# Performance work log

Measured on AMD Instinct MI355X. Metric: run time of the kernel, lower is better.

The kernel has to match this reference:

```python
import jax, jax.numpy as jnp
import numpy as np

B, W, N, L = 64, 256, 128, 64


def setup_inputs() -> dict:
    key = jax.random.key(0)
    k1, k2, k3 = jax.random.split(key, 3)
    x = jax.random.normal(k1, (B, W, L), dtype=jnp.float32)
    shapelets = jax.random.normal(k2, (N, L), dtype=jnp.float32)
    cls_w = jax.random.normal(k3, (1, N), dtype=jnp.float32) * 0.1
    cls_b = jnp.zeros((1,), dtype=jnp.float32)
    return {"x": x, "shapelets": shapelets, "cls_w": cls_w, "cls_b": cls_b}


def reference(x, shapelets, cls_w, cls_b):
    # diffs: [B, W, N, L] broadcast subtract
    diffs = x[:, :, None, :] - shapelets[None, None, :, :]
    # L2 norm over shapelet-length axis -> [B, W, N]
    discrim = jnp.sqrt(jnp.sum(diffs * diffs, axis=3))
    # min over windows -> [B, N]
    min_discrim = jnp.min(discrim, axis=1)
    # tiny classifier: Linear(N, 1) + sigmoid -> [B, 1]
    logits = min_discrim @ cls_w.T + cls_b
    return jax.nn.sigmoid(logits)
```

## Files before the change

### kernel.cpp

```cpp
#include <hip/hip_runtime.h>
#include <cfloat>
#include <cmath>

constexpr int B = 64;
constexpr int W = 256;
constexpr int N = 128;
constexpr int L = 64;
constexpr int NC = 32;
constexpr int WPB = W / NC;

__device__ int g_cnt[B];

template <int CTRL>
__device__ __forceinline__ float dpp_add(float v) {
  return v + __int_as_float(__builtin_amdgcn_update_dpp(
                 0, __float_as_int(v), CTRL, 0xF, 0xF, true));
}

__global__ __launch_bounds__(256)
void shapelet_fused_kernel(const float* __restrict__ x,
                           const float* __restrict__ shp,
                           const float* __restrict__ cls_w,
                           const float* __restrict__ cls_b,
                           float* __restrict__ part,
                           float* __restrict__ out) {
  __shared__ float xs[WPB * L];
  __shared__ float xnorm_s[WPB];
  __shared__ int s_last;
  __shared__ float red[2];

  const int b = blockIdx.x >> 5;
  const int c = blockIdx.x & 31;
  const int tid = threadIdx.x;
  const int oct = tid & 7;
  const int grp = tid >> 3;
  const int n0 = grp * 4;

  if (tid < WPB * L / 4) {
    const float4* xg =
        (const float4*)(x + ((size_t)b * W + (size_t)c * WPB) * L);
    float4 v = xg[tid];
    ((float4*)xs)[tid] = v;
    float p = v.x * v.x + v.y * v.y + v.z * v.z + v.w * v.w;
    p = dpp_add<0xB1>(p);
    p = dpp_add<0x4E>(p);
    p = dpp_add<0x141>(p);
    p = dpp_add<0x140>(p);
    if ((tid & 15) == 0) xnorm_s[tid >> 4] = p;
  }

  const float4* g0 = (const float4*)(shp + (size_t)(n0 + 0) * L + oct * 8);
  const float4* g1 = (const float4*)(shp + (size_t)(n0 + 1) * L + oct * 8);
  const float4* g2 = (const float4*)(shp + (size_t)(n0 + 2) * L + oct * 8);
  const float4* g3 = (const float4*)(shp + (size_t)(n0 + 3) * L + oct * 8);
  const float4 s0a = g0[0], s0b = g0[1];
  const float4 s1a = g1[0], s1b = g1[1];
  const float4 s2a = g2[0], s2b = g2[1];
  const float4 s3a = g3[0], s3b = g3[1];

  __syncthreads();

  float best0 = FLT_MAX, best1 = FLT_MAX, best2 = FLT_MAX, best3 = FLT_MAX;
  for (int w = 0; w < WPB; ++w) {
    const float4* xr = (const float4*)(xs + (size_t)w * L + oct * 8);
    const float4 xa = xr[0];
    const float4 xb = xr[1];

    float d0 = xa.x * s0a.x + xa.y * s0a.y;
    float d1 = xa.x * s1a.x + xa.y * s1a.y;
    float d2 = xa.x * s2a.x + xa.y * s2a.y;
    float d3 = xa.x * s3a.x + xa.y * s3a.y;
    d0 = fmaf(xa.z, s0a.z, d0); d0 = fmaf(xa.w, s0a.w, d0);
    d1 = fmaf(xa.z, s1a.z, d1); d1 = fmaf(xa.w, s1a.w, d1);
    d2 = fmaf(xa.z, s2a.z, d2); d2 = fmaf(xa.w, s2a.w, d2);
    d3 = fmaf(xa.z, s3a.z, d3); d3 = fmaf(xa.w, s3a.w, d3);
    d0 = fmaf(xb.x, s0b.x, d0); d0 = fmaf(xb.y, s0b.y, d0);
    d1 = fmaf(xb.x, s1b.x, d1); d1 = fmaf(xb.y, s1b.y, d1);
    d2 = fmaf(xb.x, s2b.x, d2); d2 = fmaf(xb.y, s2b.y, d2);
    d3 = fmaf(xb.x, s3b.x, d3); d3 = fmaf(xb.y, s3b.y, d3);
    d0 = fmaf(xb.z, s0b.z, d0); d0 = fmaf(xb.w, s0b.w, d0);
    d1 = fmaf(xb.z, s1b.z, d1); d1 = fmaf(xb.w, s1b.w, d1);
    d2 = fmaf(xb.z, s2b.z, d2); d2 = fmaf(xb.w, s2b.w, d2);
    d3 = fmaf(xb.z, s3b.z, d3); d3 = fmaf(xb.w, s3b.w, d3);

    d0 = dpp_add<0xB1>(d0);  d1 = dpp_add<0xB1>(d1);
    d2 = dpp_add<0xB1>(d2);  d3 = dpp_add<0xB1>(d3);
    d0 = dpp_add<0x4E>(d0);  d1 = dpp_add<0x4E>(d1);
    d2 = dpp_add<0x4E>(d2);  d3 = dpp_add<0x4E>(d3);
    d0 = dpp_add<0x141>(d0); d1 = dpp_add<0x141>(d1);
    d2 = dpp_add<0x141>(d2); d3 = dpp_add<0x141>(d3);

    const float xn = xnorm_s[w];
    best0 = fminf(best0, fmaf(-2.f, d0, xn));
    best1 = fminf(best1, fmaf(-2.f, d1, xn));
    best2 = fminf(best2, fmaf(-2.f, d2, xn));
    best3 = fminf(best3, fmaf(-2.f, d3, xn));
  }

  if (oct == 0) {
    float* p = part + ((size_t)b * NC + c) * N + n0;
    __hip_atomic_store(p + 0, best0, __ATOMIC_RELAXED,
                       __HIP_MEMORY_SCOPE_AGENT);
    __hip_atomic_store(p + 1, best1, __ATOMIC_RELAXED,
                       __HIP_MEMORY_SCOPE_AGENT);
    __hip_atomic_store(p + 2, best2, __ATOMIC_RELAXED,
                       __HIP_MEMORY_SCOPE_AGENT);
    __hip_atomic_store(p + 3, best3, __ATOMIC_RELAXED,
                       __HIP_MEMORY_SCOPE_AGENT);
  }

  __syncthreads();
  if (tid == 0) {
    int done = __hip_atomic_fetch_add(&g_cnt[b], 1, __ATOMIC_RELAXED,
                                      __HIP_MEMORY_SCOPE_AGENT);
    s_last = (done == NC - 1) ? 1 : 0;
    if (done == NC - 1)
      __hip_atomic_store(&g_cnt[b], 0, __ATOMIC_RELAXED,
                         __HIP_MEMORY_SCOPE_AGENT);
  }
  __syncthreads();
  if (!s_last) return;

  float v = 0.f;
  if (tid < N) {
    const float* pb = part + (size_t)b * NC * N + tid;
    float m = FLT_MAX;
#pragma unroll
    for (int cc = 0; cc < NC; ++cc) {
      float pv = __hip_atomic_load(pb + cc * N, __ATOMIC_RELAXED,
                                   __HIP_MEMORY_SCOPE_AGENT);
      m = fminf(m, pv);
    }
    float sn = 0.f;
    const float4* sg = (const float4*)(shp + (size_t)tid * L);
#pragma unroll
    for (int i = 0; i < L / 4; ++i) {
      float4 s = sg[i];
      sn = fmaf(s.x, s.x, sn);
      sn = fmaf(s.y, s.y, sn);
      sn = fmaf(s.z, s.z, sn);
      sn = fmaf(s.w, s.w, sn);
    }
    float d2 = fmaxf(m + sn, 0.f);
    v = sqrtf(d2) * cls_w[tid];
  }
#pragma unroll
  for (int off = 32; off > 0; off >>= 1) v += __shfl_down(v, off, 64);
  if ((tid & 63) == 0) red[tid >> 6] = v;
  __syncthreads();
  if (tid == 0) {
    float z = red[0] + red[1] + cls_b[0];
    out[b] = 1.0f / (1.0f + expf(-z));
  }
}

extern "C" void kernel_launch(void* const* d_in, const int* in_sizes, int n_in,
                              void* d_out, int out_size, void* d_ws,
                              size_t ws_size, hipStream_t stream) {
  const float* x = (const float*)d_in[0];
  const float* shp = (const float*)d_in[1];
  const float* cls_w = (const float*)d_in[2];
  const float* cls_b = (const float*)d_in[3];
  float* out = (float*)d_out;
  float* part = (float*)d_ws;

  shapelet_fused_kernel<<<B * NC, 256, 0, stream>>>(x, shp, cls_w, cls_b,
                                                    part, out);
}
```

Baseline: 77.99 us.

## Halve window chunks and use per-wave completion counter for final reduction

Cuts the number of window chunks per batch from 32 to 16, so each block loads 16 windows with all 256 threads and there are half as many blocks. The block-level syncthreads and counter handshake is replaced by a per-wave atomic counter; the last arriving wave does the final min, norm and classifier reduction alone. This removes two block barriers and shared-memory reduction traffic. The risk is longer per-block loops and weaker cross-wave memory ordering, since only workgroup-scope fences are used before an agent-scope counter.

After: 88.83 us. +13.9%, slower.

```diff
diff --git a/kernel.cpp b/kernel.cpp
--- a/kernel.cpp
+++ b/kernel.cpp
@@ -6,8 +6,9 @@
 constexpr int W = 256;
 constexpr int N = 128;
 constexpr int L = 64;
-constexpr int NC = 32;
+constexpr int NC = 16;
 constexpr int WPB = W / NC;
+constexpr int WAVES_PER_B = NC * 4;
 
 __device__ int g_cnt[B];
 
@@ -26,17 +27,24 @@
                            float* __restrict__ out) {
   __shared__ float xs[WPB * L];
   __shared__ float xnorm_s[WPB];
-  __shared__ int s_last;
-  __shared__ float red[2];
 
-  const int b = blockIdx.x >> 5;
-  const int c = blockIdx.x & 31;
+  const int b = blockIdx.x >> 4;
+  const int c = blockIdx.x & 15;
   const int tid = threadIdx.x;
   const int oct = tid & 7;
   const int grp = tid >> 3;
   const int n0 = grp * 4;
 
-  if (tid < WPB * L / 4) {
+  const float4* g0 = (const float4*)(shp + (size_t)(n0 + 0) * L + oct * 8);
+  const float4* g1 = (const float4*)(shp + (size_t)(n0 + 1) * L + oct * 8);
+  const float4* g2 = (const float4*)(shp + (size_t)(n0 + 2) * L + oct * 8);
+  const float4* g3 = (const float4*)(shp + (size_t)(n0 + 3) * L + oct * 8);
+  const float4 s0a = g0[0], s0b = g0[1];
+  const float4 s1a = g1[0], s1b = g1[1];
+  const float4 s2a = g2[0], s2b = g2[1];
+  const float4 s3a = g3[0], s3b = g3[1];
+
+  {
     const float4* xg =
         (const float4*)(x + ((size_t)b * W + (size_t)c * WPB) * L);
     float4 v = xg[tid];
@@ -48,15 +56,6 @@
     p = dpp_add<0x140>(p);
     if ((tid & 15) == 0) xnorm_s[tid >> 4] = p;
   }
-
-  const float4* g0 = (const float4*)(shp + (size_t)(n0 + 0) * L + oct * 8);
-  const float4* g1 = (const float4*)(shp + (size_t)(n0 + 1) * L + oct * 8);
-  const float4* g2 = (const float4*)(shp + (size_t)(n0 + 2) * L + oct * 8);
-  const float4* g3 = (const float4*)(shp + (size_t)(n0 + 3) * L + oct * 8);
-  const float4 s0a = g0[0], s0b = g0[1];
-  const float4 s1a = g1[0], s1b = g1[1];
-  const float4 s2a = g2[0], s2b = g2[1];
-  const float4 s3a = g3[0], s3b = g3[1];
 
   __syncthreads();
 
@@ -109,47 +108,54 @@
                        __HIP_MEMORY_SCOPE_AGENT);
   }
 
-  __syncthreads();
-  if (tid == 0) {
-    int done = __hip_atomic_fetch_add(&g_cnt[b], 1, __ATOMIC_RELAXED,
-                                      __HIP_MEMORY_SCOPE_AGENT);
-    s_last = (done == NC - 1) ? 1 : 0;
-    if (done == NC - 1)
-      __hip_atomic_store(&g_cnt[b], 0, __ATOMIC_RELAXED,
-                         __HIP_MEMORY_SCOPE_AGENT);
-  }
-  __syncthreads();
-  if (!s_last) return;
+  __builtin_amdgcn_fence(__ATOMIC_RELEASE, "workgroup");
+  int done = 0;
+  if ((tid & 63) == 0)
+    done = __hip_atomic_fetch_add(&g_cnt[b], 1, __ATOMIC_RELAXED,
+                                  __HIP_MEMORY_SCOPE_AGENT);
+  done = __builtin_amdgcn_readfirstlane(done);
+  if (done != WAVES_PER_B - 1) return;
 
-  float v = 0.f;
-  if (tid < N) {
-    const float* pb = part + (size_t)b * NC * N + tid;
-    float m = FLT_MAX;
+  __builtin_amdgcn_fence(__ATOMIC_ACQUIRE, "workgroup");
+  const int lane = tid & 63;
+  if (lane == 0)
+    __hip_atomic_store(&g_cnt[b], 0, __ATOMIC_RELAXED,
+                       __HIP_MEMORY_SCOPE_AGENT);
+
+  float m0 = FLT_MAX, m1 = FLT_MAX;
+  {
+    const float* pb = part + (size_t)b * NC * N + lane;
 #pragma unroll
     for (int cc = 0; cc < NC; ++cc) {
-      float pv = __hip_atomic_load(pb + cc * N, __ATOMIC_RELAXED,
+      float p0 = __hip_atomic_load(pb + cc * N, __ATOMIC_RELAXED,
                                    __HIP_MEMORY_SCOPE_AGENT);
-      m = fminf(m, pv);
+      float p1 = __hip_atomic_load(pb + cc * N + 64, __ATOMIC_RELAXED,
+                                   __HIP_MEMORY_SCOPE_AGENT);
+      m0 = fminf(m0, p0);
+      m1 = fminf(m1, p1);
     }
-    float sn = 0.f;
-    const float4* sg = (const float4*)(shp + (size_t)tid * L);
+  }
+
+  float sn0 = 0.f, sn1 = 0.f;
+  {
+    const float4* sg0 = (const float4*)(shp + (size_t)lane * L);
+    const float4* sg1 = (const float4*)(shp + (size_t)(lane + 64) * L);
 #pragma unroll
     for (int i = 0; i < L / 4; ++i) {
-      float4 s = sg[i];
-      sn = fmaf(s.x, s.x, sn);
-      sn = fmaf(s.y, s.y, sn);
-      sn = fmaf(s.z, s.z, sn);
-      sn = fmaf(s.w, s.w, sn);
+      float4 a = sg0[i], bq = sg1[i];
+      sn0 = fmaf(a.x, a.x, sn0);  sn0 = fmaf(a.y, a.y, sn0);
+      sn0 = fmaf(a.z, a.z, sn0);  sn0 = fmaf(a.w, a.w, sn0);
+      sn1 = fmaf(bq.x, bq.x, sn1); sn1 = fmaf(bq.y, bq.y, sn1);
+      sn1 = fmaf(bq.z, bq.z, sn1); sn1 = fmaf(bq.w, bq.w, sn1);
     }
-    float d2 = fmaxf(m + sn, 0.f);
-    v = sqrtf(d2) * cls_w[tid];
   }
+
+  float v = sqrtf(fmaxf(m0 + sn0, 0.f)) * cls_w[lane] +
+            sqrtf(fmaxf(m1 + sn1, 0.f)) * cls_w[lane + 64];
 #pragma unroll
   for (int off = 32; off > 0; off >>= 1) v += __shfl_down(v, off, 64);
-  if ((tid & 63) == 0) red[tid >> 6] = v;
-  __syncthreads();
-  if (tid == 0) {
-    float z = red[0] + red[1] + cls_b[0];
+  if (lane == 0) {
+    float z = v + cls_b[0];
     out[b] = 1.0f / (1.0f + expf(-z));
   }
 }
```
